# Optimization experiments

Measured on AMD Instinct MI355X. Metric: run time of the kernel, lower is better.

Reference implementation:

```python
import jax, jax.numpy as jnp
import numpy as np

D_MODEL = 1024
N_HEADS = 16
BATCH = 4
SEQ = 2048


def setup_inputs() -> dict:
    key = jax.random.key(0)
    ks = jax.random.split(key, 8)
    scale = 1.0 / np.sqrt(D_MODEL)
    q = jax.random.normal(ks[0], (BATCH, SEQ, D_MODEL), dtype=jnp.float32)
    k = jax.random.normal(ks[1], (BATCH, SEQ, D_MODEL), dtype=jnp.float32)
    v = jax.random.normal(ks[2], (BATCH, SEQ, D_MODEL), dtype=jnp.float32)
    # boolean mask: True positions are masked out (set to -1e10)
    mask = jax.random.bernoulli(ks[3], 0.1, (BATCH, N_HEADS, SEQ, SEQ))
    W_q = jax.random.normal(ks[4], (D_MODEL, D_MODEL), dtype=jnp.float32) * scale
    b_q = jnp.zeros((D_MODEL,), dtype=jnp.float32)
    W_o = jax.random.normal(ks[5], (D_MODEL, D_MODEL), dtype=jnp.float32) * scale
    b_o = jnp.zeros((D_MODEL,), dtype=jnp.float32)
    return {"q": q, "k": k, "v": v, "mask": mask,
            "W_q": W_q, "b_q": b_q, "W_o": W_o, "b_o": b_o}


def _split_heads(x):
    # [b, s, (h*d)] -> [b, h, s, d]
    b, s, dm = x.shape
    return x.reshape(b, s, N_HEADS, dm // N_HEADS).transpose(0, 2, 1, 3)


def reference(q, k, v, mask, W_q, b_q, W_o, b_o):
    # NOTE: source module (faithfully) applies fc_q to q, k AND v.
    query = _split_heads(q @ W_q + b_q)
    key = _split_heads(k @ W_q + b_q)
    value = _split_heads(v @ W_q + b_q)
    d_k = jnp.sqrt(jnp.asarray(D_MODEL / N_HEADS, dtype=query.dtype))
    scores = jnp.einsum('bhqd,bhkd->bhqk', query, key) / d_k
    scores = jnp.where(mask, jnp.asarray(-1e10, dtype=scores.dtype), scores)
    weights = jax.nn.softmax(scores, axis=-1)
    attn = jnp.einsum('bhqk,bhkd->bhqd', weights, value)
    # [b, h, s, d] -> [b, s, h*d]
    b, h, s, d = attn.shape
    attn = attn.transpose(0, 2, 1, 3).reshape(b, s, h * d)
    return attn @ W_o + b_o
```

## Files before the change

kernel.cpp:

```cpp
#include <hip/hip_runtime.h>
#include <cstdint>
#include <cstddef>

typedef __attribute__((ext_vector_type(8))) short bf16x8;
typedef __attribute__((ext_vector_type(4))) float f32x4;

static __device__ __forceinline__ short f2bf(float f){
  union { float f; unsigned u; } c; c.f = f;
  unsigned r = c.u + 0x7FFFu + ((c.u >> 16) & 1u);
  return (short)(r >> 16);
}

__global__ void detect_mask_kernel(const unsigned int* __restrict__ m, int* __restrict__ flag){
  __shared__ unsigned int red[256];
  unsigned int mx = 0u;
  for (int i = threadIdx.x; i < 16384; i += 256){ unsigned v = m[i]; if (v > mx) mx = v; }
  red[threadIdx.x] = mx;
  __syncthreads();
  for (int s = 128; s > 0; s >>= 1){
    if ((int)threadIdx.x < s){ unsigned v = red[threadIdx.x + s]; if (v > red[threadIdx.x]) red[threadIdx.x] = v; }
    __syncthreads();
  }
  if (threadIdx.x == 0){
    unsigned v = red[0];
    flag[0] = (v <= 1u) ? 1 : ((v <= 0x01010101u) ? 0 : 2);
  }
}

__global__ __launch_bounds__(256) void pack_mask_kernel(const void* __restrict__ maskp,
                                                        const int* __restrict__ flagp,
                                                        unsigned int* __restrict__ mbits){
  const int fl = *flagp;
  const size_t W = (size_t)blockIdx.x * 256 + threadIdx.x;
  unsigned int w = 0u;
  if (fl == 0){
    const uint4* p = (const uint4*)((const unsigned char*)maskp + W * 32);
    uint4 a = p[0], b = p[1];
    unsigned int arr[8] = {a.x, a.y, a.z, a.w, b.x, b.y, b.z, b.w};
    #pragma unroll
    for (int i = 0; i < 8; i++){
      unsigned int v = arr[i];
      #pragma unroll
      for (int j = 0; j < 4; j++)
        w |= (((v >> (8 * j)) & 0xffu) ? 1u : 0u) << (i * 4 + j);
    }
  } else {
    const uint4* p = (const uint4*)maskp + W * 8;
    #pragma unroll
    for (int i = 0; i < 8; i++){
      uint4 v = p[i];
      w |= (v.x ? 1u : 0u) << (i * 4 + 0);
      w |= (v.y ? 1u : 0u) << (i * 4 + 1);
      w |= (v.z ? 1u : 0u) << (i * 4 + 2);
      w |= (v.w ? 1u : 0u) << (i * 4 + 3);
    }
  }
  mbits[W] = w;
}

__global__ __launch_bounds__(256) void cast_qkv_kernel(const float* __restrict__ q,
                                                       const float* __restrict__ k,
                                                       const float* __restrict__ v,
                                                       short* __restrict__ xb){
  const int z = blockIdx.z;
  const float* src = (z == 0) ? q : ((z == 1) ? k : v);
  short* dst = xb + (size_t)z * 8388608;
  for (int u = blockIdx.x * 256 + threadIdx.x; u < 1048576; u += 512 * 256){
    const float4* s4 = (const float4*)src + (size_t)u * 2;
    float4 f0 = s4[0], f1 = s4[1];
    bf16x8 o;
    o[0] = f2bf(f0.x); o[1] = f2bf(f0.y); o[2] = f2bf(f0.z); o[3] = f2bf(f0.w);
    o[4] = f2bf(f1.x); o[5] = f2bf(f1.y); o[6] = f2bf(f1.z); o[7] = f2bf(f1.w);
    *(bf16x8*)(dst + (size_t)u * 8) = o;
  }
}

__global__ void transpose_w_kernel(const float* __restrict__ Wq, const float* __restrict__ Wo,
                                   short* __restrict__ WqT, short* __restrict__ WoT){
  __shared__ float tile[32][33];
  const float* src = blockIdx.z ? Wo : Wq;
  short* dst = blockIdx.z ? WoT : WqT;
  int x = blockIdx.x * 32 + threadIdx.x;
  int y = blockIdx.y * 32 + threadIdx.y;
  tile[threadIdx.y][threadIdx.x] = src[(size_t)y * 1024 + x];
  __syncthreads();
  int n = blockIdx.x * 32 + threadIdx.y;
  int kk = blockIdx.y * 32 + threadIdx.x;
  dst[(size_t)n * 1024 + kk] = f2bf(tile[threadIdx.x][threadIdx.y]);
}

template<int MODE>
__global__ __launch_bounds__(256) void gemm_bt_kernel(const short* __restrict__ Abase,
                                                      const short* __restrict__ Bt,
                                                      const float* __restrict__ bias,
                                                      void* __restrict__ OutBase){
  __shared__ short As[128 * 40];
  __shared__ short Bs[128 * 40];
  const int t = threadIdx.x, w = t >> 6, l = t & 63, lr = l & 15, lh = (l >> 4) & 3;
  const int wr = w >> 1, wc = w & 1;
  const int bm0 = blockIdx.y * 128, bn0 = blockIdx.x * 128;
  const size_t zoff = (size_t)blockIdx.z * 8388608;
  const short* A = Abase + zoff;

  f32x4 acc[4][4];
  #pragma unroll
  for (int i = 0; i < 4; i++)
    #pragma unroll
    for (int n = 0; n < 4; n++) acc[i][n] = (f32x4){0.f, 0.f, 0.f, 0.f};

  const int seg0 = t, seg1 = t + 256;
  const int r0 = seg0 >> 2, c0 = (seg0 & 3) * 8;
  const int r1 = seg1 >> 2, c1 = (seg1 & 3) * 8;
  const short* Ap0 = A  + (size_t)(bm0 + r0) * 1024 + c0;
  const short* Ap1 = A  + (size_t)(bm0 + r1) * 1024 + c1;
  const short* Bp0 = Bt + (size_t)(bn0 + r0) * 1024 + c0;
  const short* Bp1 = Bt + (size_t)(bn0 + r1) * 1024 + c1;

  bf16x8 pa0 = *(const bf16x8*)Ap0, pa1 = *(const bf16x8*)Ap1;
  bf16x8 pb0 = *(const bf16x8*)Bp0, pb1 = *(const bf16x8*)Bp1;

  #pragma unroll 1
  for (int k0 = 0; k0 < 1024; k0 += 32){
    __syncthreads();
    *(bf16x8*)&As[r0 * 40 + c0] = pa0; *(bf16x8*)&As[r1 * 40 + c1] = pa1;
    *(bf16x8*)&Bs[r0 * 40 + c0] = pb0; *(bf16x8*)&Bs[r1 * 40 + c1] = pb1;
    __syncthreads();
    if (k0 + 32 < 1024){
      pa0 = *(const bf16x8*)(Ap0 + k0 + 32);
      pa1 = *(const bf16x8*)(Ap1 + k0 + 32);
      pb0 = *(const bf16x8*)(Bp0 + k0 + 32);
      pb1 = *(const bf16x8*)(Bp1 + k0 + 32);
    }
    bf16x8 af[4], bg[4];
    #pragma unroll
    for (int i = 0; i < 4; i++) af[i] = *(const bf16x8*)&As[(wr * 64 + i * 16 + lr) * 40 + lh * 8];
    #pragma unroll
    for (int n = 0; n < 4; n++) bg[n] = *(const bf16x8*)&Bs[(wc * 64 + n * 16 + lr) * 40 + lh * 8];
    #pragma unroll
    for (int i = 0; i < 4; i++)
      #pragma unroll
      for (int n = 0; n < 4; n++)
        acc[i][n] = __builtin_amdgcn_mfma_f32_16x16x32_bf16(af[i], bg[n], acc[i][n], 0, 0, 0);
  }

  #pragma unroll
  for (int i = 0; i < 4; i++)
    #pragma unroll
    for (int n = 0; n < 4; n++)
      #pragma unroll
      for (int r = 0; r < 4; r++){
        int row = bm0 + wr * 64 + i * 16 + lh * 4 + r;
        int col = bn0 + wc * 64 + n * 16 + lr;
        float val = acc[i][n][r] + bias[col];
        if (MODE == 0){
          int bb = row >> 11, s = row & 2047, hh = col >> 6, dd = col & 63;
          ((short*)OutBase)[zoff + (((size_t)(bb * 16 + hh)) * 2048 + (size_t)s) * 64 + dd] = f2bf(val);
        } else {
          ((float*)OutBase)[(size_t)row * 1024 + col] = val;
        }
      }
}

__global__ __launch_bounds__(256) void attn_kernel(const short* __restrict__ P,
                                                   const unsigned int* __restrict__ mbits,
                                                   short* __restrict__ attn_out){
  constexpr int S = 2048, D = 64;
  __shared__ short Klds[64][72];
  __shared__ short Vt[64][72];
  __shared__ short Plds[4][32][72];

  const int t = threadIdx.x, w = t >> 6, l = t & 63;
  const int lr = l & 15, lh = (l >> 4) & 3;
  const int bid = blockIdx.x;
  const int xcd = bid & 7, yy = bid >> 3;
  const int bh = xcd + 8 * (yy & 7);
  const int q0 = (yy >> 3) * 128;

  const size_t headP = (size_t)bh * S * D;
  const short* Pq = P + headP;
  const short* Pk = P + (size_t)64 * S * D + headP;
  const short* Pv = P + (size_t)128 * S * D + headP;

  bf16x8 qa[2][2];
  #pragma unroll
  for (int m = 0; m < 2; m++)
    #pragma unroll
    for (int kk = 0; kk < 2; kk++){
      int row = q0 + w * 32 + m * 16 + lr;
      qa[m][kk] = *(const bf16x8*)(Pq + (size_t)row * D + kk * 32 + lh * 8);
    }

  f32x4 o[2][4];
  #pragma unroll
  for (int m = 0; m < 2; m++)
    #pragma unroll
    for (int n = 0; n < 4; n++) o[m][n] = (f32x4){0.f, 0.f, 0.f, 0.f};
  float psum[2][4];
  #pragma unroll
  for (int m = 0; m < 2; m++)
    #pragma unroll
    for (int r = 0; r < 4; r++) psum[m][r] = 0.f;

  int moff[2][4];
  #pragma unroll
  for (int m = 0; m < 2; m++)
    #pragma unroll
    for (int r = 0; r < 4; r++)
      moff[m][r] = ((bh * 2048) + q0 + w * 32 + m * 16 + lh * 4 + r) * 64;

  const int krow0 = t >> 3, kcol = (t & 7) * 8, krow1 = krow0 + 32;

  bf16x8 kreg0 = *(const bf16x8*)(Pk + (size_t)krow0 * D + kcol);
  bf16x8 kreg1 = *(const bf16x8*)(Pk + (size_t)krow1 * D + kcol);
  bf16x8 vreg0 = *(const bf16x8*)(Pv + (size_t)l * D + w * 16);
  bf16x8 vreg1 = *(const bf16x8*)(Pv + (size_t)l * D + w * 16 + 8);
  uint2 mw[2][4];
  #pragma unroll
  for (int m = 0; m < 2; m++)
    #pragma unroll
    for (int r = 0; r < 4; r++)
      mw[m][r] = *(const uint2*)(mbits + moff[m][r]);

  #pragma unroll 1
  for (int kv0 = 0; kv0 < S; kv0 += 64){
    __syncthreads();
    *(bf16x8*)&Klds[krow0][kcol] = kreg0;
    *(bf16x8*)&Klds[krow1][kcol] = kreg1;
    #pragma unroll
    for (int j = 0; j < 8; j++){
      Vt[w * 16 + j][l]     = vreg0[j];
      Vt[w * 16 + 8 + j][l] = vreg1[j];
    }
    __syncthreads();

    uint2 mcur[2][4];
    #pragma unroll
    for (int m = 0; m < 2; m++)
      #pragma unroll
      for (int r = 0; r < 4; r++) mcur[m][r] = mw[m][r];
    if (kv0 + 64 < S){
      kreg0 = *(const bf16x8*)(Pk + (size_t)(kv0 + 64 + krow0) * D + kcol);
      kreg1 = *(const bf16x8*)(Pk + (size_t)(kv0 + 64 + krow1) * D + kcol);
      vreg0 = *(const bf16x8*)(Pv + (size_t)(kv0 + 64 + l) * D + w * 16);
      vreg1 = *(const bf16x8*)(Pv + (size_t)(kv0 + 64 + l) * D + w * 16 + 8);
      const int wo = (kv0 + 64) >> 5;
      #pragma unroll
      for (int m = 0; m < 2; m++)
        #pragma unroll
        for (int r = 0; r < 4; r++)
          mw[m][r] = *(const uint2*)(mbits + moff[m][r] + wo);
    }

    f32x4 sacc[2][4];
    #pragma unroll
    for (int m = 0; m < 2; m++)
      #pragma unroll
      for (int n = 0; n < 4; n++) sacc[m][n] = (f32x4){0.f, 0.f, 0.f, 0.f};
    bf16x8 kb[4][2];
    #pragma unroll
    for (int n = 0; n < 4; n++)
      #pragma unroll
      for (int kk = 0; kk < 2; kk++)
        kb[n][kk] = *(const bf16x8*)&Klds[n * 16 + lr][kk * 32 + lh * 8];
    #pragma unroll
    for (int m = 0; m < 2; m++)
      #pragma unroll
      for (int n = 0; n < 4; n++)
        #pragma unroll
        for (int kk = 0; kk < 2; kk++)
          sacc[m][n] = __builtin_amdgcn_mfma_f32_16x16x32_bf16(qa[m][kk], kb[n][kk], sacc[m][n], 0, 0, 0);

    #pragma unroll
    for (int m = 0; m < 2; m++)
      #pragma unroll
      for (int n = 0; n < 4; n++){
        const unsigned wsel = (n < 2) ? 0u : 1u;
        const int bitpos = (n & 1) * 16 + lr;
        #pragma unroll
        for (int r = 0; r < 4; r++){
          unsigned word = wsel ? mcur[m][r].y : mcur[m][r].x;
          bool msk = (word >> bitpos) & 1u;
          float p = msk ? 0.f : exp2f(fmaf(sacc[m][n][r], 0.18033688f, -17.3123405f));
          psum[m][r] += p;
          Plds[w][m * 16 + lh * 4 + r][n * 16 + lr] = f2bf(p);
        }
      }

    bf16x8 pa[2][2], vb[4][2];
    #pragma unroll
    for (int m = 0; m < 2; m++)
      #pragma unroll
      for (int kk = 0; kk < 2; kk++)
        pa[m][kk] = *(const bf16x8*)&Plds[w][m * 16 + lr][kk * 32 + lh * 8];
    #pragma unroll
    for (int n = 0; n < 4; n++)
      #pragma unroll
      for (int kk = 0; kk < 2; kk++)
        vb[n][kk] = *(const bf16x8*)&Vt[n * 16 + lr][kk * 32 + lh * 8];
    #pragma unroll
    for (int m = 0; m < 2; m++)
      #pragma unroll
      for (int n = 0; n < 4; n++)
        #pragma unroll
        for (int kk = 0; kk < 2; kk++)
          o[m][n] = __builtin_amdgcn_mfma_f32_16x16x32_bf16(pa[m][kk], vb[n][kk], o[m][n], 0, 0, 0);
  }

  float lrow[2][4];
  #pragma unroll
  for (int m = 0; m < 2; m++)
    #pragma unroll
    for (int r = 0; r < 4; r++){
      float s = psum[m][r];
      s += __shfl_xor(s, 1);
      s += __shfl_xor(s, 2);
      s += __shfl_xor(s, 4);
      s += __shfl_xor(s, 8);
      lrow[m][r] = s;
    }

  const int b = bh >> 4, h = bh & 15;
  #pragma unroll
  for (int m = 0; m < 2; m++)
    #pragma unroll
    for (int n = 0; n < 4; n++)
      #pragma unroll
      for (int r = 0; r < 4; r++){
        int qrow = q0 + w * 32 + m * 16 + lh * 4 + r;
        int d = n * 16 + lr;
        float val = o[m][n][r] / lrow[m][r];
        attn_out[((size_t)(b * S + qrow)) * 1024 + h * 64 + d] = f2bf(val);
      }
}

extern "C" void kernel_launch(void* const* d_in, const int* in_sizes, int n_in,
                              void* d_out, int out_size, void* d_ws, size_t ws_size,
                              hipStream_t stream){
  const float* q    = (const float*)d_in[0];
  const float* k    = (const float*)d_in[1];
  const float* v    = (const float*)d_in[2];
  const void*  mask = d_in[3];
  const float* Wq   = (const float*)d_in[4];
  const float* bq   = (const float*)d_in[5];
  const float* Wo   = (const float*)d_in[6];
  const float* bo   = (const float*)d_in[7];

  short* ws_s = (short*)d_ws;
  short* Xb   = ws_s;
  short* WqT  = ws_s + 25165824;
  short* WoT  = WqT + 1048576;
  short* Pp   = WoT + 1048576;
  int*   flag = (int*)(Pp + 25165824);
  short* attn_ws = ws_s;
  unsigned int* mbits = (unsigned int*)(ws_s + 8388608);

  detect_mask_kernel<<<1, 256, 0, stream>>>((const unsigned int*)mask, flag);
  cast_qkv_kernel<<<dim3(512, 1, 3), 256, 0, stream>>>(q, k, v, Xb);
  transpose_w_kernel<<<dim3(32, 32, 2), dim3(32, 32), 0, stream>>>(Wq, Wo, WqT, WoT);
  gemm_bt_kernel<0><<<dim3(8, 64, 3), 256, 0, stream>>>(Xb, WqT, bq, (void*)Pp);
  pack_mask_kernel<<<32768, 256, 0, stream>>>(mask, flag, mbits);
  attn_kernel<<<1024, 256, 0, stream>>>(Pp, mbits, attn_ws);
  gemm_bt_kernel<1><<<dim3(8, 64, 1), 256, 0, stream>>>(attn_ws, WoT, bo, d_out);
}
```

Baseline: 1.760 ms.

## Load GEMM tiles directly into LDS and regroup attention blocks by head

The projection GEMM now stages A and B tiles with global_load_lds direct-to-LDS transfers, dropping the register prefetch and the padded LDS layout. The load is no longer overlapped with compute, and the unpadded stride of 32 may add LDS bank conflicts. The attention kernel's block-index mapping is changed so the 16 query tiles of a head land on the same XCD consecutively, aiming for better L2 reuse of K and V.

```diff
diff --git a/kernel.cpp b/kernel.cpp
--- a/kernel.cpp
+++ b/kernel.cpp
@@ -9,6 +9,11 @@
   union { float f; unsigned u; } c; c.f = f;
   unsigned r = c.u + 0x7FFFu + ((c.u >> 16) & 1u);
   return (short)(r >> 16);
+}
+
+static __device__ __forceinline__ void gload16(const void* g, void* l){
+  __builtin_amdgcn_global_load_lds((const __attribute__((address_space(1))) void*)g,
+                                   (__attribute__((address_space(3))) void*)l, 16, 0, 0);
 }
 
 __global__ void detect_mask_kernel(const unsigned int* __restrict__ m, int* __restrict__ flag){
@@ -94,8 +99,8 @@
                                                       const short* __restrict__ Bt,
                                                       const float* __restrict__ bias,
                                                       void* __restrict__ OutBase){
-  __shared__ short As[128 * 40];
-  __shared__ short Bs[128 * 40];
+  __shared__ short As[128 * 32];
+  __shared__ short Bs[128 * 32];
   const int t = threadIdx.x, w = t >> 6, l = t & 63, lr = l & 15, lh = (l >> 4) & 3;
   const int wr = w >> 1, wc = w & 1;
   const int bm0 = blockIdx.y * 128, bn0 = blockIdx.x * 128;
@@ -108,34 +113,24 @@
     #pragma unroll
     for (int n = 0; n < 4; n++) acc[i][n] = (f32x4){0.f, 0.f, 0.f, 0.f};
 
-  const int seg0 = t, seg1 = t + 256;
-  const int r0 = seg0 >> 2, c0 = (seg0 & 3) * 8;
-  const int r1 = seg1 >> 2, c1 = (seg1 & 3) * 8;
-  const short* Ap0 = A  + (size_t)(bm0 + r0) * 1024 + c0;
-  const short* Ap1 = A  + (size_t)(bm0 + r1) * 1024 + c1;
-  const short* Bp0 = Bt + (size_t)(bn0 + r0) * 1024 + c0;
-  const short* Bp1 = Bt + (size_t)(bn0 + r1) * 1024 + c1;
-
-  bf16x8 pa0 = *(const bf16x8*)Ap0, pa1 = *(const bf16x8*)Ap1;
-  bf16x8 pb0 = *(const bf16x8*)Bp0, pb1 = *(const bf16x8*)Bp1;
+  const int srow = l >> 2;
+  const int scol = (l & 3) * 8;
 
   #pragma unroll 1
   for (int k0 = 0; k0 < 1024; k0 += 32){
     __syncthreads();
-    *(bf16x8*)&As[r0 * 40 + c0] = pa0; *(bf16x8*)&As[r1 * 40 + c1] = pa1;
-    *(bf16x8*)&Bs[r0 * 40 + c0] = pb0; *(bf16x8*)&Bs[r1 * 40 + c1] = pb1;
-    __syncthreads();
-    if (k0 + 32 < 1024){
-      pa0 = *(const bf16x8*)(Ap0 + k0 + 32);
-      pa1 = *(const bf16x8*)(Ap1 + k0 + 32);
-      pb0 = *(const bf16x8*)(Bp0 + k0 + 32);
-      pb1 = *(const bf16x8*)(Bp1 + k0 + 32);
-    }
+    #pragma unroll
+    for (int j = 0; j < 2; j++){
+      const int R = w * 32 + j * 16;
+      gload16(A  + (size_t)(bm0 + R + srow) * 1024 + k0 + scol, &As[R * 32]);
+      gload16(Bt + (size_t)(bn0 + R + srow) * 1024 + k0 + scol, &Bs[R * 32]);
+    }
+    __syncthreads();
     bf16x8 af[4], bg[4];
     #pragma unroll
-    for (int i = 0; i < 4; i++) af[i] = *(const bf16x8*)&As[(wr * 64 + i * 16 + lr) * 40 + lh * 8];
-    #pragma unroll
-    for (int n = 0; n < 4; n++) bg[n] = *(const bf16x8*)&Bs[(wc * 64 + n * 16 + lr) * 40 + lh * 8];
+    for (int i = 0; i < 4; i++) af[i] = *(const bf16x8*)&As[(wr * 64 + i * 16 + lr) * 32 + lh * 8];
+    #pragma unroll
+    for (int n = 0; n < 4; n++) bg[n] = *(const bf16x8*)&Bs[(wc * 64 + n * 16 + lr) * 32 + lh * 8];
     #pragma unroll
     for (int i = 0; i < 4; i++)
       #pragma unroll
@@ -172,9 +167,12 @@
   const int t = threadIdx.x, w = t >> 6, l = t & 63;
   const int lr = l & 15, lh = (l >> 4) & 3;
   const int bid = blockIdx.x;
-  const int xcd = bid & 7, yy = bid >> 3;
-  const int bh = xcd + 8 * (yy & 7);
-  const int q0 = (yy >> 3) * 128;
+  const int c   = bid & 7;
+  const int rem = bid >> 3;
+  const int m16 = rem & 15;
+  const int g   = rem >> 4;
+  const int bh  = c + 8 * g;
+  const int q0  = m16 * 128;
 
   const size_t headP = (size_t)bh * S * D;
   const short* Pq = P + headP;
```

After: 1.776 ms. About the same (+0.9%).
